# Kernel tuning notes

Measured on AMD Instinct MI355X. Metric: run time of the kernel, lower is better.

## Reference

```python
import jax, jax.numpy as jnp
import numpy as np

V, DH, E, KV = 30, 512, 256, 128  # vocab, decoder hidden, embed (=2*KV, tied), key/value dim
B, T, L = 256, 800, 300
SOS = 0


def _lstm_cell(x, h, c, w_ih, w_hh, b_ih, b_hh):
    g = x @ w_ih.T + b_ih + h @ w_hh.T + b_hh
    i, f, gg, o = jnp.split(g, 4, axis=-1)
    i, f, o = jax.nn.sigmoid(i), jax.nn.sigmoid(f), jax.nn.sigmoid(o)
    c2 = f * c + i * jnp.tanh(gg)
    return o * jnp.tanh(c2), c2


def setup_inputs() -> dict:
    key = jax.random.key(0)
    ks = jax.random.split(key, 12)
    emb = 0.1 * jax.random.normal(ks[0], (V, E), jnp.float32)
    emb = emb.at[0].set(0.0)  # padding_idx=0
    return {
        "key_enc": jax.random.normal(ks[1], (B, T, KV), jnp.float32),
        "value": jax.random.normal(ks[2], (B, T, KV), jnp.float32),
        "encoder_len": jax.random.randint(ks[3], (B,), 100, T + 1, jnp.int32),
        "y": jax.random.randint(ks[4], (B, L), 0, V, jnp.int64),
        "embedding": emb,  # also the tied character_prob weight (V, 2*KV)
        "w_ih1": 0.05 * jax.random.normal(ks[5], (4 * DH, E + KV), jnp.float32),
        "w_hh1": 0.05 * jax.random.normal(ks[6], (4 * DH, DH), jnp.float32),
        "b_ih1": jnp.zeros((4 * DH,), jnp.float32),
        "b_hh1": jnp.zeros((4 * DH,), jnp.float32),
        "w_ih2": 0.05 * jax.random.normal(ks[7], (4 * KV, DH), jnp.float32),
        "w_hh2": 0.05 * jax.random.normal(ks[8], (4 * KV, KV), jnp.float32),
        "b_ih2": jnp.zeros((4 * KV,), jnp.float32),
        "b_hh2": jnp.zeros((4 * KV,), jnp.float32),
        "out_bias": jnp.zeros((V,), jnp.float32),
    }


def reference(key_enc, value, encoder_len, y, embedding,
              w_ih1, w_hh1, b_ih1, b_hh1, w_ih2, w_hh2, b_ih2, b_hh2, out_bias):
    Bb, Tt, _ = key_enc.shape
    max_len = y.shape[1]
    valid = jnp.arange(Tt)[None, :] < encoder_len[:, None]  # (B, T)

    # teacher-forced embeddings: <sos> then y[:, :-1]
    sos = jnp.broadcast_to(embedding[SOS], (Bb, E))
    embeds = jnp.concatenate([sos[:, None, :], embedding[y[:, :-1]]], axis=1)  # (B, L, E)
    embeds = jnp.transpose(embeds, (1, 0, 2))  # (L, B, E)

    z1 = jnp.zeros((Bb, DH), key_enc.dtype)
    z2 = jnp.zeros((Bb, KV), key_enc.dtype)
    init = (z1, z1, z2, z2, value[:, 0, :])

    def step(carry, emb):
        h1, c1, h2, c2, ctx = carry
        x = jnp.concatenate([emb, ctx], axis=1)
        h1, c1 = _lstm_cell(x, h1, c1, w_ih1, w_hh1, b_ih1, b_hh1)
        h2, c2 = _lstm_cell(h1, h2, c2, w_ih2, w_hh2, b_ih2, b_hh2)
        q = h2  # (B, KV)
        energy = jnp.einsum('btk,bk->bt', key_enc, q)
        energy = jnp.where(valid, energy, -1e9)
        attn = jax.nn.softmax(energy, axis=-1)
        ctx = jnp.einsum('bt,btk->bk', attn, value)
        pred = jnp.concatenate([q, ctx], axis=1) @ embedding.T + out_bias  # tied weights
        return (h1, c1, h2, c2, ctx), (pred, attn[0])

    _, (preds, attn_plot) = jax.lax.scan(step, init, embeds)
    predictions = jnp.transpose(preds, (1, 0, 2))  # (B, L, V)
    return predictions, attn_plot  # attn_plot: (L, T)
```

## Files before the change

kernel.cpp:

```cpp
#include <hip/hip_runtime.h>
#include <cstddef>

#define NV   30
#define NDH  512
#define NE   256
#define NKV  128
#define NB   256
#define NT   800
#define NL   300
#define NKX  896

#define PRED_SIZE (NB*NL*NV)

typedef float v4f __attribute__((ext_vector_type(4)));
typedef short bf16x8 __attribute__((ext_vector_type(8)));
typedef unsigned short ushort_t;

#define OFF_C1   0
#define OFF_C2   131072
#define OFF_H2F  163840
#define OFF_XB   196608
#define OFF_XH2  458752
#define OFF_WF   524288
#define OFF_WF2  2359296
#define OFF_BS1  2686976
#define OFF_BS2  2689024

#define WF_PL   ((size_t)128*28*64*8)
#define WF2_PL  ((size_t)32*20*64*8)

struct DecParams {
  const float* key; const float* val; const int* elen; const int* y;
  const float* emb;
  const float* wi1; const float* wh1; const float* bi1; const float* bh1;
  const float* wi2; const float* wh2; const float* bi2; const float* bh2;
  const float* ob;
  float* out; float* ws;
};

__device__ __forceinline__ float sigm(float x)  { return 1.0f/(1.0f + __expf(-x)); }
__device__ __forceinline__ float tanh_f(float x){ return 1.0f - 2.0f/(__expf(2.0f*x)+1.0f); }

__device__ __forceinline__ ushort_t bf16_rne(float x){
  union { float f; unsigned u; } v; v.f = x;
  unsigned r = v.u + 0x7FFFu + ((v.u >> 16) & 1u);
  return (ushort_t)(r >> 16);
}
__device__ __forceinline__ float bf16_to_f(ushort_t h){
  union { float f; unsigned u; } v; v.u = ((unsigned)h) << 16;
  return v.f;
}

__global__ void __launch_bounds__(256)
k_init(DecParams P)
{
  P.ws[blockIdx.x * 256 + threadIdx.x] = 0.0f;
}

__global__ void __launch_bounds__(256)
k_initX(DecParams P)
{
  const int b = blockIdx.x, tid = threadIdx.x;
  if (tid < 128) {
    ushort_t* xbh = (ushort_t*)(P.ws + OFF_XB);
    ushort_t* xbl = xbh + (size_t)256*1024;
    const float v = P.val[(size_t)b*NT*NKV + tid];
    const ushort_t hi = bf16_rne(v);
    const ushort_t lo = bf16_rne(v - bf16_to_f(hi));
    xbh[(size_t)b*1024 + 256 + tid] = hi;
    xbl[(size_t)b*1024 + 256 + tid] = lo;
  }
}

__global__ void __launch_bounds__(256)
k_initW(DecParams P)
{
  const int r = blockIdx.x;
  const int tid = threadIdx.x;
  ushort_t* wf = (ushort_t*)(P.ws + OFF_WF);
  const int rt = r >> 4;
#pragma unroll
  for (int i = 0; i < 4; ++i) {
    const int k = i*256 + tid;
    if (k < NKX) {
      const float w = (k < 384) ? P.wi1[(size_t)r*384 + k]
                                : P.wh1[(size_t)r*512 + (k - 384)];
      const ushort_t hi = bf16_rne(w);
      const ushort_t lo = bf16_rne(w - bf16_to_f(hi));
      const int kc = k >> 5;
      const int lane = (r & 15) | (((k >> 3) & 3) << 4);
      const int e = k & 7;
      const size_t base = ((((size_t)rt)*28 + kc)*64 + lane)*8 + e;
      wf[base] = hi;
      wf[WF_PL + base] = lo;
    }
  }
  if (tid == 0) P.ws[OFF_BS1 + r] = P.bi1[r] + P.bh1[r];
}

__global__ void __launch_bounds__(256)
k_initW2(DecParams P)
{
  const int r = blockIdx.x;
  const int tid = threadIdx.x;
  ushort_t* wf = (ushort_t*)(P.ws + OFF_WF2);
  const int rt = r >> 4;
#pragma unroll
  for (int i = 0; i < 3; ++i) {
    const int k = i*256 + tid;
    if (k < 640) {
      const float w = (k < 512) ? P.wi2[(size_t)r*512 + k]
                                : P.wh2[(size_t)r*128 + (k - 512)];
      const ushort_t hi = bf16_rne(w);
      const ushort_t lo = bf16_rne(w - bf16_to_f(hi));
      const int kc = k >> 5;
      const int lane = (r & 15) | (((k >> 3) & 3) << 4);
      const int e = k & 7;
      const size_t base = ((((size_t)rt)*20 + kc)*64 + lane)*8 + e;
      wf[base] = hi;
      wf[WF2_PL + base] = lo;
    }
  }
  if (tid == 0) P.ws[OFF_BS2 + r] = P.bi2[r] + P.bh2[r];
}

__global__ void __launch_bounds__(256)
k_stepA(DecParams P)
{
  __shared__ ushort_t xs[2][32][136];
  __shared__ float gbuf[4][16][33];
  const int tid = threadIdx.x, bid = blockIdx.x;
  const int mt = bid & 31, nt = bid >> 5;
  const int b0 = nt * 32, j0 = mt * 16;
  const int w = tid >> 6, lane = tid & 63;
  const int rt16 = w*32 + mt;

  const ushort_t* Wf  = (const ushort_t*)(P.ws + OFF_WF);
  const ushort_t* XbH = (const ushort_t*)(P.ws + OFF_XB);
  const ushort_t* XbL = XbH + (size_t)256*1024;
  float* C1 = P.ws + OFF_C1;
  const float* BS1 = P.ws + OFF_BS1;

  v4f acc[2] = {(v4f)0.0f, (v4f)0.0f};
  const int srow = tid >> 3, sk = (tid & 7) * 16;
  const int lr = lane & 15, lk8 = (lane >> 4) * 8;

#pragma unroll 1
  for (int p = 0; p < 7; ++p) {
    __syncthreads();
    {
      const ushort_t* s0 = XbH + (size_t)(b0 + srow)*1024 + p*128 + sk;
      const ushort_t* s1 = XbL + (size_t)(b0 + srow)*1024 + p*128 + sk;
      *(bf16x8*)&xs[0][srow][sk]     = ((const bf16x8*)s0)[0];
      *(bf16x8*)&xs[0][srow][sk + 8] = ((const bf16x8*)s0)[1];
      *(bf16x8*)&xs[1][srow][sk]     = ((const bf16x8*)s1)[0];
      *(bf16x8*)&xs[1][srow][sk + 8] = ((const bf16x8*)s1)[1];
    }
    __syncthreads();
#pragma unroll
    for (int kc2 = 0; kc2 < 4; ++kc2) {
      const int kcg = p*4 + kc2;
      bf16x8 ah = *(const bf16x8*)(Wf + (((size_t)rt16*28 + kcg)*64 + lane)*8);
      bf16x8 al = *(const bf16x8*)(Wf + WF_PL + (((size_t)rt16*28 + kcg)*64 + lane)*8);
      const int lk = kc2*32 + lk8;
#pragma unroll
      for (int ct = 0; ct < 2; ++ct) {
        bf16x8 bh = *(const bf16x8*)&xs[0][ct*16 + lr][lk];
        bf16x8 bl = *(const bf16x8*)&xs[1][ct*16 + lr][lk];
        acc[ct] = __builtin_amdgcn_mfma_f32_16x16x32_bf16(ah, bh, acc[ct], 0, 0, 0);
        acc[ct] = __builtin_amdgcn_mfma_f32_16x16x32_bf16(ah, bl, acc[ct], 0, 0, 0);
        acc[ct] = __builtin_amdgcn_mfma_f32_16x16x32_bf16(al, bh, acc[ct], 0, 0, 0);
      }
    }
  }
  __syncthreads();
  const int rg = (lane >> 4) * 4;
#pragma unroll
  for (int ct = 0; ct < 2; ++ct)
#pragma unroll
    for (int j = 0; j < 4; ++j)
      gbuf[w][rg + j][ct*16 + lr] = acc[ct][j];
  __syncthreads();

  ushort_t* XbHw = (ushort_t*)(P.ws + OFF_XB);
  ushort_t* XbLw = XbHw + (size_t)256*1024;
#pragma unroll
  for (int it = 0; it < 2; ++it) {
    const int idx = it*256 + tid;
    const int jj = idx >> 5, bq = idx & 31;
    const int jg = j0 + jj, b = b0 + bq;
    const float iv = sigm (gbuf[0][jj][bq] + BS1[       jg]);
    const float fv = sigm (gbuf[1][jj][bq] + BS1[ 512 + jg]);
    const float gv = tanh_f(gbuf[2][jj][bq] + BS1[1024 + jg]);
    const float ov = sigm (gbuf[3][jj][bq] + BS1[1536 + jg]);
    const float cn = fv * C1[(size_t)jg*256 + b] + iv * gv;
    C1[(size_t)jg*256 + b] = cn;
    const float h = ov * tanh_f(cn);
    const ushort_t hi = bf16_rne(h);
    const ushort_t lo = bf16_rne(h - bf16_to_f(hi));
    XbHw[(size_t)b*1024 + 384 + jg] = hi;
    XbLw[(size_t)b*1024 + 384 + jg] = lo;
  }
}

__global__ void __launch_bounds__(256)
k_stepB(DecParams P, int t)
{
  __shared__ ushort_t xs[2][32][136];
  __shared__ float gbuf[4][16][33];
  const int tid = threadIdx.x, bid = blockIdx.x;
  const int mt = bid & 7, nt = bid >> 3;
  const int b0 = nt * 32, j0 = mt * 16;
  const int w = tid >> 6, lane = tid & 63;
  const int rt16 = w*8 + mt;

  const ushort_t* Wf2 = (const ushort_t*)(P.ws + OFF_WF2);
  const ushort_t* XbH = (const ushort_t*)(P.ws + OFF_XB);
  const ushort_t* XbL = XbH + (size_t)256*1024;
  const ushort_t* XH2 = (const ushort_t*)(P.ws + OFF_XH2);
  float* C2  = P.ws + OFF_C2;
  float* H2f = P.ws + OFF_H2F;
  const float* BS2 = P.ws + OFF_BS2;
  const int pp = t & 1, pn = (t + 1) & 1;

  v4f acc[2] = {(v4f)0.0f, (v4f)0.0f};
  const int srow = tid >> 3, sk = (tid & 7) * 16;
  const int lr = lane & 15, lk8 = (lane >> 4) * 8;

#pragma unroll 1
  for (int p = 0; p < 5; ++p) {
    __syncthreads();
    {
      const ushort_t* s0;
      const ushort_t* s1;
      if (p < 4) {
        s0 = XbH + (size_t)(b0 + srow)*1024 + 384 + p*128 + sk;
        s1 = XbL + (size_t)(b0 + srow)*1024 + 384 + p*128 + sk;
      } else {
        s0 = XH2 + ((size_t)(pp*2 + 0)*256 + b0 + srow)*128 + sk;
        s1 = XH2 + ((size_t)(pp*2 + 1)*256 + b0 + srow)*128 + sk;
      }
      *(bf16x8*)&xs[0][srow][sk]     = ((const bf16x8*)s0)[0];
      *(bf16x8*)&xs[0][srow][sk + 8] = ((const bf16x8*)s0)[1];
      *(bf16x8*)&xs[1][srow][sk]     = ((const bf16x8*)s1)[0];
      *(bf16x8*)&xs[1][srow][sk + 8] = ((const bf16x8*)s1)[1];
    }
    __syncthreads();
#pragma unroll
    for (int kc2 = 0; kc2 < 4; ++kc2) {
      const int kcg = p*4 + kc2;
      bf16x8 ah = *(const bf16x8*)(Wf2 + (((size_t)rt16*20 + kcg)*64 + lane)*8);
      bf16x8 al = *(const bf16x8*)(Wf2 + WF2_PL + (((size_t)rt16*20 + kcg)*64 + lane)*8);
      const int lk = kc2*32 + lk8;
#pragma unroll
      for (int ct = 0; ct < 2; ++ct) {
        bf16x8 bh = *(const bf16x8*)&xs[0][ct*16 + lr][lk];
        bf16x8 bl = *(const bf16x8*)&xs[1][ct*16 + lr][lk];
        acc[ct] = __builtin_amdgcn_mfma_f32_16x16x32_bf16(ah, bh, acc[ct], 0, 0, 0);
        acc[ct] = __builtin_amdgcn_mfma_f32_16x16x32_bf16(ah, bl, acc[ct], 0, 0, 0);
        acc[ct] = __builtin_amdgcn_mfma_f32_16x16x32_bf16(al, bh, acc[ct], 0, 0, 0);
      }
    }
  }
  __syncthreads();
  const int rg = (lane >> 4) * 4;
#pragma unroll
  for (int ct = 0; ct < 2; ++ct)
#pragma unroll
    for (int j = 0; j < 4; ++j)
      gbuf[w][rg + j][ct*16 + lr] = acc[ct][j];
  __syncthreads();

  ushort_t* XH2w = (ushort_t*)(P.ws + OFF_XH2);
#pragma unroll
  for (int it = 0; it < 2; ++it) {
    const int idx = it*256 + tid;
    const int jj = idx >> 5, bq = idx & 31;
    const int j2 = j0 + jj, b = b0 + bq;
    const float iv = sigm (gbuf[0][jj][bq] + BS2[      j2]);
    const float fv = sigm (gbuf[1][jj][bq] + BS2[128 + j2]);
    const float gv = tanh_f(gbuf[2][jj][bq] + BS2[256 + j2]);
    const float ov = sigm (gbuf[3][jj][bq] + BS2[384 + j2]);
    const float cn = fv * C2[(size_t)j2*256 + b] + iv * gv;
    C2[(size_t)j2*256 + b] = cn;
    const float h = ov * tanh_f(cn);
    H2f[(size_t)b*128 + j2] = h;
    const ushort_t hi = bf16_rne(h);
    const ushort_t lo = bf16_rne(h - bf16_to_f(hi));
    XH2w[((size_t)(pn*2 + 0)*256 + b)*128 + j2] = hi;
    XH2w[((size_t)(pn*2 + 1)*256 + b)*128 + j2] = lo;
  }
}

__global__ void __launch_bounds__(512)
k_stepC(DecParams P, int t)
{
  __shared__ float e[NT];
  __shared__ float qc[256];
  __shared__ float red[16];
  __shared__ float ctxp[16][132];

  const int tid = threadIdx.x;
  const int b = blockIdx.x;
  const int len = P.elen[b];
  const float* H2f = P.ws + OFF_H2F;
  ushort_t* xbh = (ushort_t*)(P.ws + OFF_XB);
  ushort_t* xbl = xbh + (size_t)256*1024;

  if (tid < 128) qc[tid] = H2f[(size_t)b*128 + tid];
  __syncthreads();

  const int lg = tid & 15, grp = tid >> 4;
  const v4f qa = *(const v4f*)&qc[lg*8];
  const v4f qb = *(const v4f*)&qc[lg*8 + 4];
  const v4f* kb = (const v4f*)(P.key + (size_t)b*NT*NKV);
#pragma unroll 1
  for (int s = 0; s < 13; ++s) {
    const int ta = s*64 + grp, tb = ta + 32;
    float pa = 0.0f, pb = 0.0f;
    if (ta < len) {
      v4f k0 = kb[(size_t)ta*32 + lg*2], k1 = kb[(size_t)ta*32 + lg*2 + 1];
      v4f d = k0*qa + k1*qb; pa = d[0]+d[1]+d[2]+d[3];
    }
    if (tb < len) {
      v4f k0 = kb[(size_t)tb*32 + lg*2], k1 = kb[(size_t)tb*32 + lg*2 + 1];
      v4f d = k0*qa + k1*qb; pb = d[0]+d[1]+d[2]+d[3];
    }
    pa += __shfl_xor(pa, 1); pb += __shfl_xor(pb, 1);
    pa += __shfl_xor(pa, 2); pb += __shfl_xor(pb, 2);
    pa += __shfl_xor(pa, 4); pb += __shfl_xor(pb, 4);
    pa += __shfl_xor(pa, 8); pb += __shfl_xor(pb, 8);
    if (lg == 0) {
      if (ta < len) e[ta] = pa;
      if (tb < len) e[tb] = pb;
    }
  }
  for (int tt = len + tid; tt < NT; tt += 512) e[tt] = -1e9f;
  __syncthreads();

  const int wid = tid >> 6;
  const float x0 = e[tid];
  const float x1 = (tid < NT - 512) ? e[512 + tid] : -3.0e38f;
  float m = fmaxf(x0, x1);
  m = fmaxf(m, __shfl_xor(m, 1));  m = fmaxf(m, __shfl_xor(m, 2));
  m = fmaxf(m, __shfl_xor(m, 4));  m = fmaxf(m, __shfl_xor(m, 8));
  m = fmaxf(m, __shfl_xor(m, 16)); m = fmaxf(m, __shfl_xor(m, 32));
  if ((tid & 63) == 0) red[wid] = m;
  __syncthreads();
  m = red[0];
#pragma unroll
  for (int i = 1; i < 8; ++i) m = fmaxf(m, red[i]);
  const float p0 = __expf(x0 - m);
  const float p1 = (tid < NT - 512) ? __expf(x1 - m) : 0.0f;
  float ss = p0 + p1;
  ss += __shfl_xor(ss, 1);  ss += __shfl_xor(ss, 2);  ss += __shfl_xor(ss, 4);
  ss += __shfl_xor(ss, 8);  ss += __shfl_xor(ss, 16); ss += __shfl_xor(ss, 32);
  if ((tid & 63) == 0) red[8 + wid] = ss;
  __syncthreads();
  float S = red[8];
#pragma unroll
  for (int i = 1; i < 8; ++i) S += red[8 + i];
  const float inv = 1.0f / S;
  e[tid] = p0 * inv;
  if (tid < NT - 512) e[512 + tid] = p1 * inv;
  if (b == 0) {
    P.out[PRED_SIZE + (size_t)t*NT + tid] = p0 * inv;
    if (tid < NT - 512) P.out[PRED_SIZE + (size_t)t*NT + 512 + tid] = p1 * inv;
  }
  __syncthreads();

  {
    const int kq = tid & 31, tq = tid >> 5;
    const v4f* vb = (const v4f*)(P.val + (size_t)b*NT*NKV);
    v4f a4 = (v4f)0.0f, a42 = (v4f)0.0f;
    int tt = tq;
    for (; tt + 16 < len; tt += 32) {
      a4  += e[tt]      * vb[(size_t)tt*32 + kq];
      a42 += e[tt + 16] * vb[(size_t)(tt + 16)*32 + kq];
    }
    if (tt < len) a4 += e[tt] * vb[(size_t)tt*32 + kq];
    a4 += a42;
    *(v4f*)&ctxp[tq][kq*4] = a4;
  }
  __syncthreads();
  if (tid < 128) {
    const int k = tid;
    float c = 0.0f;
#pragma unroll
    for (int r = 0; r < 16; ++r) c += ctxp[r][k];
    qc[128 + k] = c;
    const ushort_t hi = bf16_rne(c);
    const ushort_t lo = bf16_rne(c - bf16_to_f(hi));
    xbh[(size_t)b*1024 + 256 + k] = hi;
    xbl[(size_t)b*1024 + 256 + k] = lo;
  }
  __syncthreads();

  {
    const int vv = tid >> 4, lg16 = tid & 15;
    if (vv < NV) {
      const v4f* er = (const v4f*)(P.emb + (size_t)vv*NE + lg16*16);
      const v4f* qr = (const v4f*)&qc[lg16*16];
      v4f s4 = er[0]*qr[0] + er[1]*qr[1] + er[2]*qr[2] + er[3]*qr[3];
      float p = s4[0] + s4[1] + s4[2] + s4[3];
      p += __shfl_xor(p, 1); p += __shfl_xor(p, 2);
      p += __shfl_xor(p, 4); p += __shfl_xor(p, 8);
      if (lg16 == 0) P.out[((size_t)b*NL + t)*NV + vv] = p + P.ob[vv];
    }
  }

  if (tid < 256) {
    const int tok = P.y[(size_t)b*NL + t];
    const float x = P.emb[(size_t)tok*NE + tid];
    const ushort_t hi = bf16_rne(x);
    const ushort_t lo = bf16_rne(x - bf16_to_f(hi));
    xbh[(size_t)b*1024 + tid] = hi;
    xbl[(size_t)b*1024 + tid] = lo;
  }
}

extern "C" void kernel_launch(void* const* d_in, const int* in_sizes, int n_in,
                              void* d_out, int out_size, void* d_ws, size_t ws_size,
                              hipStream_t stream) {
  (void)in_sizes; (void)n_in; (void)out_size; (void)ws_size;
  DecParams P;
  P.key  = (const float*)d_in[0];
  P.val  = (const float*)d_in[1];
  P.elen = (const int*)d_in[2];
  P.y    = (const int*)d_in[3];
  P.emb  = (const float*)d_in[4];
  P.wi1  = (const float*)d_in[5];
  P.wh1  = (const float*)d_in[6];
  P.bi1  = (const float*)d_in[7];
  P.bh1  = (const float*)d_in[8];
  P.wi2  = (const float*)d_in[9];
  P.wh2  = (const float*)d_in[10];
  P.bi2  = (const float*)d_in[11];
  P.bh2  = (const float*)d_in[12];
  P.ob   = (const float*)d_in[13];
  P.out  = (float*)d_out;
  P.ws   = (float*)d_ws;

  hipLaunchKernelGGL(k_init,   dim3(2048), dim3(256), 0, stream, P);
  hipLaunchKernelGGL(k_initX,  dim3(256),  dim3(256), 0, stream, P);
  hipLaunchKernelGGL(k_initW,  dim3(2048), dim3(256), 0, stream, P);
  hipLaunchKernelGGL(k_initW2, dim3(512),  dim3(256), 0, stream, P);
  for (int t = 0; t < NL; ++t) {
    hipLaunchKernelGGL(k_stepA, dim3(256), dim3(256), 0, stream, P);
    hipLaunchKernelGGL(k_stepB, dim3(64),  dim3(256), 0, stream, P, t);
    hipLaunchKernelGGL(k_stepC, dim3(NB),  dim3(512), 0, stream, P, t);
  }
}
```

Before: 15.61 ms.

## Fuse per-step kernels into a persistent kernel with grid barriers

Replaces the 900 per-timestep launches of three kernels with one persistent kernel that loops over timesteps and separates the LSTM1, LSTM2 and attention phases with a software grid barrier. The workspace layout is split into separate embed/context and double-buffered h1/h2 buffers so phases can read the previous step's state. Blocks grow to 512 threads, with each wave owning one column tile. The aim is to remove launch overhead and inter-kernel gaps, at the cost of atomic spin-barrier latency, a timeout fallback that flags failure, and the risk of deadlock if the computed grid is not fully co-resident.

After: 53.87 ms. 3.45x slower.

```diff
diff --git a/kernel.cpp b/kernel.cpp
--- a/kernel.cpp
+++ b/kernel.cpp
@@ -19,12 +19,14 @@
 #define OFF_C1   0
 #define OFF_C2   131072
 #define OFF_H2F  163840
-#define OFF_XB   196608
-#define OFF_XH2  458752
-#define OFF_WF   524288
-#define OFF_WF2  2359296
-#define OFF_BS1  2686976
-#define OFF_BS2  2689024
+#define OFF_XEC  196608
+#define OFF_XH1  294912
+#define OFF_XH2  557056
+#define OFF_BAR  622592
+#define OFF_WF   622848
+#define OFF_WF2  2457856
+#define OFF_BS1  2785536
+#define OFF_BS2  2787584
 
 #define WF_PL   ((size_t)128*28*64*8)
 #define WF2_PL  ((size_t)32*20*64*8)
@@ -51,6 +53,32 @@
   return v.f;
 }
 
+__device__ __forceinline__ void gridbar(int* bar, int G)
+{
+  __syncthreads();
+  if (threadIdx.x == 0) {
+    __threadfence_system();
+    const int g = __hip_atomic_load(&bar[1], __ATOMIC_RELAXED, __HIP_MEMORY_SCOPE_SYSTEM);
+    const int v = __hip_atomic_fetch_add(&bar[0], 1, __ATOMIC_ACQ_REL, __HIP_MEMORY_SCOPE_SYSTEM);
+    if (v == G - 1) {
+      __hip_atomic_store(&bar[0], 0, __ATOMIC_RELAXED, __HIP_MEMORY_SCOPE_SYSTEM);
+      __hip_atomic_fetch_add(&bar[1], 1, __ATOMIC_ACQ_REL, __HIP_MEMORY_SCOPE_SYSTEM);
+    } else {
+      long spins = 0;
+      while (__hip_atomic_load(&bar[1], __ATOMIC_ACQUIRE, __HIP_MEMORY_SCOPE_SYSTEM) == g) {
+        __builtin_amdgcn_s_sleep(8);
+        if (++spins > (1L << 20)) {
+          __hip_atomic_store(&bar[2], 1, __ATOMIC_RELAXED, __HIP_MEMORY_SCOPE_SYSTEM);
+          break;
+        }
+        if (__hip_atomic_load(&bar[2], __ATOMIC_RELAXED, __HIP_MEMORY_SCOPE_SYSTEM)) break;
+      }
+    }
+    __threadfence_system();
+  }
+  __syncthreads();
+}
+
 __global__ void __launch_bounds__(256)
 k_init(DecParams P)
 {
@@ -62,13 +90,12 @@
 {
   const int b = blockIdx.x, tid = threadIdx.x;
   if (tid < 128) {
-    ushort_t* xbh = (ushort_t*)(P.ws + OFF_XB);
-    ushort_t* xbl = xbh + (size_t)256*1024;
+    ushort_t* xec = (ushort_t*)(P.ws + OFF_XEC);
     const float v = P.val[(size_t)b*NT*NKV + tid];
     const ushort_t hi = bf16_rne(v);
     const ushort_t lo = bf16_rne(v - bf16_to_f(hi));
-    xbh[(size_t)b*1024 + 256 + tid] = hi;
-    xbl[(size_t)b*1024 + 256 + tid] = lo;
+    xec[((size_t)0*256 + b)*384 + 256 + tid] = hi;
+    xec[((size_t)1*256 + b)*384 + 256 + tid] = lo;
   }
 }
 
@@ -124,298 +151,286 @@
   if (tid == 0) P.ws[OFF_BS2 + r] = P.bi2[r] + P.bh2[r];
 }
 
-__global__ void __launch_bounds__(256)
-k_stepA(DecParams P)
-{
-  __shared__ ushort_t xs[2][32][136];
-  __shared__ float gbuf[4][16][33];
-  const int tid = threadIdx.x, bid = blockIdx.x;
-  const int mt = bid & 31, nt = bid >> 5;
-  const int b0 = nt * 32, j0 = mt * 16;
+union SMem {
+  struct { ushort_t xs[2][32][136]; float gbuf[4][16][33]; } ab;
+  struct { float e[NT]; float qc[256]; float red[16]; float ctxp[16][132]; } c;
+};
+
+__global__ void __launch_bounds__(512)
+k_persist(DecParams P, int G)
+{
+  __shared__ SMem sm;
+  const int tid = threadIdx.x;
+  const int bid = blockIdx.x;
   const int w = tid >> 6, lane = tid & 63;
-  const int rt16 = w*32 + mt;
-
-  const ushort_t* Wf  = (const ushort_t*)(P.ws + OFF_WF);
-  const ushort_t* XbH = (const ushort_t*)(P.ws + OFF_XB);
-  const ushort_t* XbL = XbH + (size_t)256*1024;
-  float* C1 = P.ws + OFF_C1;
-  const float* BS1 = P.ws + OFF_BS1;
-
-  v4f acc[2] = {(v4f)0.0f, (v4f)0.0f};
-  const int srow = tid >> 3, sk = (tid & 7) * 16;
   const int lr = lane & 15, lk8 = (lane >> 4) * 8;
-
-#pragma unroll 1
-  for (int p = 0; p < 7; ++p) {
-    __syncthreads();
-    {
-      const ushort_t* s0 = XbH + (size_t)(b0 + srow)*1024 + p*128 + sk;
-      const ushort_t* s1 = XbL + (size_t)(b0 + srow)*1024 + p*128 + sk;
-      *(bf16x8*)&xs[0][srow][sk]     = ((const bf16x8*)s0)[0];
-      *(bf16x8*)&xs[0][srow][sk + 8] = ((const bf16x8*)s0)[1];
-      *(bf16x8*)&xs[1][srow][sk]     = ((const bf16x8*)s1)[0];
-      *(bf16x8*)&xs[1][srow][sk + 8] = ((const bf16x8*)s1)[1];
-    }
-    __syncthreads();
-#pragma unroll
-    for (int kc2 = 0; kc2 < 4; ++kc2) {
-      const int kcg = p*4 + kc2;
-      bf16x8 ah = *(const bf16x8*)(Wf + (((size_t)rt16*28 + kcg)*64 + lane)*8);
-      bf16x8 al = *(const bf16x8*)(Wf + WF_PL + (((size_t)rt16*28 + kcg)*64 + lane)*8);
-      const int lk = kc2*32 + lk8;
-#pragma unroll
-      for (int ct = 0; ct < 2; ++ct) {
-        bf16x8 bh = *(const bf16x8*)&xs[0][ct*16 + lr][lk];
-        bf16x8 bl = *(const bf16x8*)&xs[1][ct*16 + lr][lk];
-        acc[ct] = __builtin_amdgcn_mfma_f32_16x16x32_bf16(ah, bh, acc[ct], 0, 0, 0);
-        acc[ct] = __builtin_amdgcn_mfma_f32_16x16x32_bf16(ah, bl, acc[ct], 0, 0, 0);
-        acc[ct] = __builtin_amdgcn_mfma_f32_16x16x32_bf16(al, bh, acc[ct], 0, 0, 0);
-      }
-    }
-  }
-  __syncthreads();
-  const int rg = (lane >> 4) * 4;
-#pragma unroll
-  for (int ct = 0; ct < 2; ++ct)
-#pragma unroll
-    for (int j = 0; j < 4; ++j)
-      gbuf[w][rg + j][ct*16 + lr] = acc[ct][j];
-  __syncthreads();
-
-  ushort_t* XbHw = (ushort_t*)(P.ws + OFF_XB);
-  ushort_t* XbLw = XbHw + (size_t)256*1024;
-#pragma unroll
-  for (int it = 0; it < 2; ++it) {
-    const int idx = it*256 + tid;
-    const int jj = idx >> 5, bq = idx & 31;
-    const int jg = j0 + jj, b = b0 + bq;
-    const float iv = sigm (gbuf[0][jj][bq] + BS1[       jg]);
-    const float fv = sigm (gbuf[1][jj][bq] + BS1[ 512 + jg]);
-    const float gv = tanh_f(gbuf[2][jj][bq] + BS1[1024 + jg]);
-    const float ov = sigm (gbuf[3][jj][bq] + BS1[1536 + jg]);
-    const float cn = fv * C1[(size_t)jg*256 + b] + iv * gv;
-    C1[(size_t)jg*256 + b] = cn;
-    const float h = ov * tanh_f(cn);
-    const ushort_t hi = bf16_rne(h);
-    const ushort_t lo = bf16_rne(h - bf16_to_f(hi));
-    XbHw[(size_t)b*1024 + 384 + jg] = hi;
-    XbLw[(size_t)b*1024 + 384 + jg] = lo;
-  }
-}
-
-__global__ void __launch_bounds__(256)
-k_stepB(DecParams P, int t)
-{
-  __shared__ ushort_t xs[2][32][136];
-  __shared__ float gbuf[4][16][33];
-  const int tid = threadIdx.x, bid = blockIdx.x;
-  const int mt = bid & 7, nt = bid >> 3;
-  const int b0 = nt * 32, j0 = mt * 16;
-  const int w = tid >> 6, lane = tid & 63;
-  const int rt16 = w*8 + mt;
-
-  const ushort_t* Wf2 = (const ushort_t*)(P.ws + OFF_WF2);
-  const ushort_t* XbH = (const ushort_t*)(P.ws + OFF_XB);
-  const ushort_t* XbL = XbH + (size_t)256*1024;
-  const ushort_t* XH2 = (const ushort_t*)(P.ws + OFF_XH2);
-  float* C2  = P.ws + OFF_C2;
-  float* H2f = P.ws + OFF_H2F;
-  const float* BS2 = P.ws + OFF_BS2;
-  const int pp = t & 1, pn = (t + 1) & 1;
-
-  v4f acc[2] = {(v4f)0.0f, (v4f)0.0f};
-  const int srow = tid >> 3, sk = (tid & 7) * 16;
-  const int lr = lane & 15, lk8 = (lane >> 4) * 8;
-
-#pragma unroll 1
-  for (int p = 0; p < 5; ++p) {
-    __syncthreads();
-    {
-      const ushort_t* s0;
-      const ushort_t* s1;
-      if (p < 4) {
-        s0 = XbH + (size_t)(b0 + srow)*1024 + 384 + p*128 + sk;
-        s1 = XbL + (size_t)(b0 + srow)*1024 + 384 + p*128 + sk;
-      } else {
-        s0 = XH2 + ((size_t)(pp*2 + 0)*256 + b0 + srow)*128 + sk;
-        s1 = XH2 + ((size_t)(pp*2 + 1)*256 + b0 + srow)*128 + sk;
-      }
-      *(bf16x8*)&xs[0][srow][sk]     = ((const bf16x8*)s0)[0];
-      *(bf16x8*)&xs[0][srow][sk + 8] = ((const bf16x8*)s0)[1];
-      *(bf16x8*)&xs[1][srow][sk]     = ((const bf16x8*)s1)[0];
-      *(bf16x8*)&xs[1][srow][sk + 8] = ((const bf16x8*)s1)[1];
-    }
-    __syncthreads();
-#pragma unroll
-    for (int kc2 = 0; kc2 < 4; ++kc2) {
-      const int kcg = p*4 + kc2;
-      bf16x8 ah = *(const bf16x8*)(Wf2 + (((size_t)rt16*20 + kcg)*64 + lane)*8);
-      bf16x8 al = *(const bf16x8*)(Wf2 + WF2_PL + (((size_t)rt16*20 + kcg)*64 + lane)*8);
-      const int lk = kc2*32 + lk8;
-#pragma unroll
-      for (int ct = 0; ct < 2; ++ct) {
-        bf16x8 bh = *(const bf16x8*)&xs[0][ct*16 + lr][lk];
-        bf16x8 bl = *(const bf16x8*)&xs[1][ct*16 + lr][lk];
-        acc[ct] = __builtin_amdgcn_mfma_f32_16x16x32_bf16(ah, bh, acc[ct], 0, 0, 0);
-        acc[ct] = __builtin_amdgcn_mfma_f32_16x16x32_bf16(ah, bl, acc[ct], 0, 0, 0);
-        acc[ct] = __builtin_amdgcn_mfma_f32_16x16x32_bf16(al, bh, acc[ct], 0, 0, 0);
-      }
-    }
-  }
-  __syncthreads();
-  const int rg = (lane >> 4) * 4;
-#pragma unroll
-  for (int ct = 0; ct < 2; ++ct)
-#pragma unroll
-    for (int j = 0; j < 4; ++j)
-      gbuf[w][rg + j][ct*16 + lr] = acc[ct][j];
-  __syncthreads();
-
-  ushort_t* XH2w = (ushort_t*)(P.ws + OFF_XH2);
-#pragma unroll
-  for (int it = 0; it < 2; ++it) {
-    const int idx = it*256 + tid;
-    const int jj = idx >> 5, bq = idx & 31;
-    const int j2 = j0 + jj, b = b0 + bq;
-    const float iv = sigm (gbuf[0][jj][bq] + BS2[      j2]);
-    const float fv = sigm (gbuf[1][jj][bq] + BS2[128 + j2]);
-    const float gv = tanh_f(gbuf[2][jj][bq] + BS2[256 + j2]);
-    const float ov = sigm (gbuf[3][jj][bq] + BS2[384 + j2]);
-    const float cn = fv * C2[(size_t)j2*256 + b] + iv * gv;
-    C2[(size_t)j2*256 + b] = cn;
-    const float h = ov * tanh_f(cn);
-    H2f[(size_t)b*128 + j2] = h;
-    const ushort_t hi = bf16_rne(h);
-    const ushort_t lo = bf16_rne(h - bf16_to_f(hi));
-    XH2w[((size_t)(pn*2 + 0)*256 + b)*128 + j2] = hi;
-    XH2w[((size_t)(pn*2 + 1)*256 + b)*128 + j2] = lo;
-  }
-}
-
-__global__ void __launch_bounds__(512)
-k_stepC(DecParams P, int t)
-{
-  __shared__ float e[NT];
-  __shared__ float qc[256];
-  __shared__ float red[16];
-  __shared__ float ctxp[16][132];
-
-  const int tid = threadIdx.x;
-  const int b = blockIdx.x;
-  const int len = P.elen[b];
-  const float* H2f = P.ws + OFF_H2F;
-  ushort_t* xbh = (ushort_t*)(P.ws + OFF_XB);
-  ushort_t* xbl = xbh + (size_t)256*1024;
-
-  if (tid < 128) qc[tid] = H2f[(size_t)b*128 + tid];
-  __syncthreads();
-
-  const int lg = tid & 15, grp = tid >> 4;
-  const v4f qa = *(const v4f*)&qc[lg*8];
-  const v4f qb = *(const v4f*)&qc[lg*8 + 4];
-  const v4f* kb = (const v4f*)(P.key + (size_t)b*NT*NKV);
-#pragma unroll 1
-  for (int s = 0; s < 13; ++s) {
-    const int ta = s*64 + grp, tb = ta + 32;
-    float pa = 0.0f, pb = 0.0f;
-    if (ta < len) {
-      v4f k0 = kb[(size_t)ta*32 + lg*2], k1 = kb[(size_t)ta*32 + lg*2 + 1];
-      v4f d = k0*qa + k1*qb; pa = d[0]+d[1]+d[2]+d[3];
-    }
-    if (tb < len) {
-      v4f k0 = kb[(size_t)tb*32 + lg*2], k1 = kb[(size_t)tb*32 + lg*2 + 1];
-      v4f d = k0*qa + k1*qb; pb = d[0]+d[1]+d[2]+d[3];
-    }
-    pa += __shfl_xor(pa, 1); pb += __shfl_xor(pb, 1);
-    pa += __shfl_xor(pa, 2); pb += __shfl_xor(pb, 2);
-    pa += __shfl_xor(pa, 4); pb += __shfl_xor(pb, 4);
-    pa += __shfl_xor(pa, 8); pb += __shfl_xor(pb, 8);
-    if (lg == 0) {
-      if (ta < len) e[ta] = pa;
-      if (tb < len) e[tb] = pb;
-    }
-  }
-  for (int tt = len + tid; tt < NT; tt += 512) e[tt] = -1e9f;
-  __syncthreads();
-
-  const int wid = tid >> 6;
-  const float x0 = e[tid];
-  const float x1 = (tid < NT - 512) ? e[512 + tid] : -3.0e38f;
-  float m = fmaxf(x0, x1);
-  m = fmaxf(m, __shfl_xor(m, 1));  m = fmaxf(m, __shfl_xor(m, 2));
-  m = fmaxf(m, __shfl_xor(m, 4));  m = fmaxf(m, __shfl_xor(m, 8));
-  m = fmaxf(m, __shfl_xor(m, 16)); m = fmaxf(m, __shfl_xor(m, 32));
-  if ((tid & 63) == 0) red[wid] = m;
-  __syncthreads();
-  m = red[0];
-#pragma unroll
-  for (int i = 1; i < 8; ++i) m = fmaxf(m, red[i]);
-  const float p0 = __expf(x0 - m);
-  const float p1 = (tid < NT - 512) ? __expf(x1 - m) : 0.0f;
-  float ss = p0 + p1;
-  ss += __shfl_xor(ss, 1);  ss += __shfl_xor(ss, 2);  ss += __shfl_xor(ss, 4);
-  ss += __shfl_xor(ss, 8);  ss += __shfl_xor(ss, 16); ss += __shfl_xor(ss, 32);
-  if ((tid & 63) == 0) red[8 + wid] = ss;
-  __syncthreads();
-  float S = red[8];
-#pragma unroll
-  for (int i = 1; i < 8; ++i) S += red[8 + i];
-  const float inv = 1.0f / S;
-  e[tid] = p0 * inv;
-  if (tid < NT - 512) e[512 + tid] = p1 * inv;
-  if (b == 0) {
-    P.out[PRED_SIZE + (size_t)t*NT + tid] = p0 * inv;
-    if (tid < NT - 512) P.out[PRED_SIZE + (size_t)t*NT + 512 + tid] = p1 * inv;
-  }
-  __syncthreads();
-
-  {
-    const int kq = tid & 31, tq = tid >> 5;
-    const v4f* vb = (const v4f*)(P.val + (size_t)b*NT*NKV);
-    v4f a4 = (v4f)0.0f, a42 = (v4f)0.0f;
-    int tt = tq;
-    for (; tt + 16 < len; tt += 32) {
-      a4  += e[tt]      * vb[(size_t)tt*32 + kq];
-      a42 += e[tt + 16] * vb[(size_t)(tt + 16)*32 + kq];
-    }
-    if (tt < len) a4 += e[tt] * vb[(size_t)tt*32 + kq];
-    a4 += a42;
-    *(v4f*)&ctxp[tq][kq*4] = a4;
-  }
-  __syncthreads();
-  if (tid < 128) {
-    const int k = tid;
-    float c = 0.0f;
-#pragma unroll
-    for (int r = 0; r < 16; ++r) c += ctxp[r][k];
-    qc[128 + k] = c;
-    const ushort_t hi = bf16_rne(c);
-    const ushort_t lo = bf16_rne(c - bf16_to_f(hi));
-    xbh[(size_t)b*1024 + 256 + k] = hi;
-    xbl[(size_t)b*1024 + 256 + k] = lo;
-  }
-  __syncthreads();
-
-  {
-    const int vv = tid >> 4, lg16 = tid & 15;
-    if (vv < NV) {
-      const v4f* er = (const v4f*)(P.emb + (size_t)vv*NE + lg16*16);
-      const v4f* qr = (const v4f*)&qc[lg16*16];
-      v4f s4 = er[0]*qr[0] + er[1]*qr[1] + er[2]*qr[2] + er[3]*qr[3];
-      float p = s4[0] + s4[1] + s4[2] + s4[3];
-      p += __shfl_xor(p, 1); p += __shfl_xor(p, 2);
-      p += __shfl_xor(p, 4); p += __shfl_xor(p, 8);
-      if (lg16 == 0) P.out[((size_t)b*NL + t)*NV + vv] = p + P.ob[vv];
-    }
-  }
-
-  if (tid < 256) {
-    const int tok = P.y[(size_t)b*NL + t];
-    const float x = P.emb[(size_t)tok*NE + tid];
-    const ushort_t hi = bf16_rne(x);
-    const ushort_t lo = bf16_rne(x - bf16_to_f(hi));
-    xbh[(size_t)b*1024 + tid] = hi;
-    xbl[(size_t)b*1024 + tid] = lo;
+  const int srow = tid >> 4, sk = (tid & 15) * 8;
+
+  float* ws = P.ws;
+  int* bar = (int*)(ws + OFF_BAR);
+  const ushort_t* Wf  = (const ushort_t*)(ws + OFF_WF);
+  const ushort_t* Wf2 = (const ushort_t*)(ws + OFF_WF2);
+  ushort_t* XEC = (ushort_t*)(ws + OFF_XEC);
+  ushort_t* XH1 = (ushort_t*)(ws + OFF_XH1);
+  ushort_t* XH2 = (ushort_t*)(ws + OFF_XH2);
+  float* C1  = ws + OFF_C1;
+  float* C2  = ws + OFF_C2;
+  float* H2f = ws + OFF_H2F;
+  const float* BS1 = ws + OFF_BS1;
+  const float* BS2 = ws + OFF_BS2;
+
+#pragma unroll 1
+  for (int t = 0; t < NL; ++t) {
+    const int cur = t & 1, nxt = (t + 1) & 1;
+
+#pragma unroll 1
+    for (int tileA = bid; tileA < 256; tileA += G) {
+      const int mt = tileA & 31, nt = tileA >> 5;
+      const int b0 = nt * 32, j0 = mt * 16;
+      const int g = w >> 1, ct = w & 1;
+      const int rt16 = g*32 + mt;
+      v4f acc = (v4f)0.0f;
+
+#pragma unroll 1
+      for (int p = 0; p < 7; ++p) {
+        __syncthreads();
+        {
+          const ushort_t *s0, *s1;
+          if (p < 3) {
+            s0 = XEC + ((size_t)(0*256 + b0 + srow))*384 + p*128 + sk;
+            s1 = XEC + ((size_t)(1*256 + b0 + srow))*384 + p*128 + sk;
+          } else {
+            s0 = XH1 + (((size_t)cur*2 + 0)*256 + b0 + srow)*512 + (p-3)*128 + sk;
+            s1 = XH1 + (((size_t)cur*2 + 1)*256 + b0 + srow)*512 + (p-3)*128 + sk;
+          }
+          *(bf16x8*)&sm.ab.xs[0][srow][sk] = *(const bf16x8*)s0;
+          *(bf16x8*)&sm.ab.xs[1][srow][sk] = *(const bf16x8*)s1;
+        }
+        __syncthreads();
+#pragma unroll
+        for (int kc2 = 0; kc2 < 4; ++kc2) {
+          const int kcg = p*4 + kc2;
+          bf16x8 ah = *(const bf16x8*)(Wf + (((size_t)rt16*28 + kcg)*64 + lane)*8);
+          bf16x8 al = *(const bf16x8*)(Wf + WF_PL + (((size_t)rt16*28 + kcg)*64 + lane)*8);
+          const int lk = kc2*32 + lk8;
+          bf16x8 bh = *(const bf16x8*)&sm.ab.xs[0][ct*16 + lr][lk];
+          bf16x8 bl = *(const bf16x8*)&sm.ab.xs[1][ct*16 + lr][lk];
+          acc = __builtin_amdgcn_mfma_f32_16x16x32_bf16(ah, bh, acc, 0, 0, 0);
+          acc = __builtin_amdgcn_mfma_f32_16x16x32_bf16(ah, bl, acc, 0, 0, 0);
+          acc = __builtin_amdgcn_mfma_f32_16x16x32_bf16(al, bh, acc, 0, 0, 0);
+        }
+      }
+      __syncthreads();
+      {
+        const int rg = (lane >> 4) * 4;
+#pragma unroll
+        for (int j = 0; j < 4; ++j) sm.ab.gbuf[g][rg + j][ct*16 + lr] = acc[j];
+      }
+      __syncthreads();
+      {
+        const int jj = tid >> 5, bq = tid & 31;
+        const int jg = j0 + jj, b = b0 + bq;
+        const float iv = sigm (sm.ab.gbuf[0][jj][bq] + BS1[       jg]);
+        const float fv = sigm (sm.ab.gbuf[1][jj][bq] + BS1[ 512 + jg]);
+        const float gv = tanh_f(sm.ab.gbuf[2][jj][bq] + BS1[1024 + jg]);
+        const float ov = sigm (sm.ab.gbuf[3][jj][bq] + BS1[1536 + jg]);
+        const float cn = fv * C1[(size_t)jg*256 + b] + iv * gv;
+        C1[(size_t)jg*256 + b] = cn;
+        const float h = ov * tanh_f(cn);
+        const ushort_t hi = bf16_rne(h);
+        const ushort_t lo = bf16_rne(h - bf16_to_f(hi));
+        XH1[(((size_t)nxt*2 + 0)*256 + b)*512 + jg] = hi;
+        XH1[(((size_t)nxt*2 + 1)*256 + b)*512 + jg] = lo;
+      }
+    }
+    gridbar(bar, G);
+
+#pragma unroll 1
+    for (int tileB = bid; tileB < 64; tileB += G) {
+      const int mt = tileB & 7, nt = tileB >> 3;
+      const int b0 = nt * 32, j0 = mt * 16;
+      const int g = w >> 1, ct = w & 1;
+      const int rt16 = g*8 + mt;
+      v4f acc = (v4f)0.0f;
+
+#pragma unroll 1
+      for (int p = 0; p < 5; ++p) {
+        __syncthreads();
+        {
+          const ushort_t *s0, *s1;
+          if (p < 4) {
+            s0 = XH1 + (((size_t)nxt*2 + 0)*256 + b0 + srow)*512 + p*128 + sk;
+            s1 = XH1 + (((size_t)nxt*2 + 1)*256 + b0 + srow)*512 + p*128 + sk;
+          } else {
+            s0 = XH2 + (((size_t)cur*2 + 0)*256 + b0 + srow)*128 + sk;
+            s1 = XH2 + (((size_t)cur*2 + 1)*256 + b0 + srow)*128 + sk;
+          }
+          *(bf16x8*)&sm.ab.xs[0][srow][sk] = *(const bf16x8*)s0;
+          *(bf16x8*)&sm.ab.xs[1][srow][sk] = *(const bf16x8*)s1;
+        }
+        __syncthreads();
+#pragma unroll
+        for (int kc2 = 0; kc2 < 4; ++kc2) {
+          const int kcg = p*4 + kc2;
+          bf16x8 ah = *(const bf16x8*)(Wf2 + (((size_t)rt16*20 + kcg)*64 + lane)*8);
+          bf16x8 al = *(const bf16x8*)(Wf2 + WF2_PL + (((size_t)rt16*20 + kcg)*64 + lane)*8);
+          const int lk = kc2*32 + lk8;
+          bf16x8 bh = *(const bf16x8*)&sm.ab.xs[0][ct*16 + lr][lk];
+          bf16x8 bl = *(const bf16x8*)&sm.ab.xs[1][ct*16 + lr][lk];
+          acc = __builtin_amdgcn_mfma_f32_16x16x32_bf16(ah, bh, acc, 0, 0, 0);
+          acc = __builtin_amdgcn_mfma_f32_16x16x32_bf16(ah, bl, acc, 0, 0, 0);
+          acc = __builtin_amdgcn_mfma_f32_16x16x32_bf16(al, bh, acc, 0, 0, 0);
+        }
+      }
+      __syncthreads();
+      {
+        const int rg = (lane >> 4) * 4;
+#pragma unroll
+        for (int j = 0; j < 4; ++j) sm.ab.gbuf[g][rg + j][ct*16 + lr] = acc[j];
+      }
+      __syncthreads();
+      {
+        const int jj = tid >> 5, bq = tid & 31;
+        const int j2 = j0 + jj, b = b0 + bq;
+        const float iv = sigm (sm.ab.gbuf[0][jj][bq] + BS2[      j2]);
+        const float fv = sigm (sm.ab.gbuf[1][jj][bq] + BS2[128 + j2]);
+        const float gv = tanh_f(sm.ab.gbuf[2][jj][bq] + BS2[256 + j2]);
+        const float ov = sigm (sm.ab.gbuf[3][jj][bq] + BS2[384 + j2]);
+        const float cn = fv * C2[(size_t)j2*256 + b] + iv * gv;
+        C2[(size_t)j2*256 + b] = cn;
+        const float h = ov * tanh_f(cn);
+        H2f[(size_t)b*128 + j2] = h;
+        const ushort_t hi = bf16_rne(h);
+        const ushort_t lo = bf16_rne(h - bf16_to_f(hi));
+        XH2[(((size_t)nxt*2 + 0)*256 + b)*128 + j2] = hi;
+        XH2[(((size_t)nxt*2 + 1)*256 + b)*128 + j2] = lo;
+      }
+    }
+    gridbar(bar, G);
+
+#pragma unroll 1
+    for (int b = bid; b < NB; b += G) {
+      __syncthreads();
+      const int len = P.elen[b];
+
+      if (tid < 128) sm.c.qc[tid] = H2f[(size_t)b*128 + tid];
+      __syncthreads();
+
+      const int lg = tid & 15, grp = tid >> 4;
+      const v4f qa = *(const v4f*)&sm.c.qc[lg*8];
+      const v4f qb = *(const v4f*)&sm.c.qc[lg*8 + 4];
+      const v4f* kb = (const v4f*)(P.key + (size_t)b*NT*NKV);
+#pragma unroll 1
+      for (int s = 0; s < 13; ++s) {
+        const int ta = s*64 + grp, tb = ta + 32;
+        float pa = 0.0f, pb = 0.0f;
+        if (ta < len) {
+          v4f k0 = kb[(size_t)ta*32 + lg*2], k1 = kb[(size_t)ta*32 + lg*2 + 1];
+          v4f d = k0*qa + k1*qb; pa = d[0]+d[1]+d[2]+d[3];
+        }
+        if (tb < len) {
+          v4f k0 = kb[(size_t)tb*32 + lg*2], k1 = kb[(size_t)tb*32 + lg*2 + 1];
+          v4f d = k0*qa + k1*qb; pb = d[0]+d[1]+d[2]+d[3];
+        }
+        pa += __shfl_xor(pa, 1); pb += __shfl_xor(pb, 1);
+        pa += __shfl_xor(pa, 2); pb += __shfl_xor(pb, 2);
+        pa += __shfl_xor(pa, 4); pb += __shfl_xor(pb, 4);
+        pa += __shfl_xor(pa, 8); pb += __shfl_xor(pb, 8);
+        if (lg == 0) {
+          if (ta < len) sm.c.e[ta] = pa;
+          if (tb < len) sm.c.e[tb] = pb;
+        }
+      }
+      for (int tt = len + tid; tt < NT; tt += 512) sm.c.e[tt] = -1e9f;
+      __syncthreads();
+
+      const int wid = tid >> 6;
+      const float x0 = sm.c.e[tid];
+      const float x1 = (tid < NT - 512) ? sm.c.e[512 + tid] : -3.0e38f;
+      float m = fmaxf(x0, x1);
+      m = fmaxf(m, __shfl_xor(m, 1));  m = fmaxf(m, __shfl_xor(m, 2));
+      m = fmaxf(m, __shfl_xor(m, 4));  m = fmaxf(m, __shfl_xor(m, 8));
+      m = fmaxf(m, __shfl_xor(m, 16)); m = fmaxf(m, __shfl_xor(m, 32));
+      if ((tid & 63) == 0) sm.c.red[wid] = m;
+      __syncthreads();
+      m = sm.c.red[0];
+#pragma unroll
+      for (int i = 1; i < 8; ++i) m = fmaxf(m, sm.c.red[i]);
+      const float p0 = __expf(x0 - m);
+      const float p1 = (tid < NT - 512) ? __expf(x1 - m) : 0.0f;
+      float ssum = p0 + p1;
+      ssum += __shfl_xor(ssum, 1);  ssum += __shfl_xor(ssum, 2);  ssum += __shfl_xor(ssum, 4);
+      ssum += __shfl_xor(ssum, 8);  ssum += __shfl_xor(ssum, 16); ssum += __shfl_xor(ssum, 32);
+      __syncthreads();
+      if ((tid & 63) == 0) sm.c.red[8 + wid] = ssum;
+      __syncthreads();
+      float S = sm.c.red[8];
+#pragma unroll
+      for (int i = 1; i < 8; ++i) S += sm.c.red[8 + i];
+      const float inv = 1.0f / S;
+      sm.c.e[tid] = p0 * inv;
+      if (tid < NT - 512) sm.c.e[512 + tid] = p1 * inv;
+      if (b == 0) {
+        P.out[PRED_SIZE + (size_t)t*NT + tid] = p0 * inv;
+        if (tid < NT - 512) P.out[PRED_SIZE + (size_t)t*NT + 512 + tid] = p1 * inv;
+      }
+      __syncthreads();
+
+      {
+        const int kq = tid & 31, tq = tid >> 5;
+        const v4f* vb = (const v4f*)(P.val + (size_t)b*NT*NKV);
+        v4f a4 = (v4f)0.0f, a42 = (v4f)0.0f;
+        int tt = tq;
+        for (; tt + 16 < len; tt += 32) {
+          a4  += sm.c.e[tt]      * vb[(size_t)tt*32 + kq];
+          a42 += sm.c.e[tt + 16] * vb[(size_t)(tt + 16)*32 + kq];
+        }
+        if (tt < len) a4 += sm.c.e[tt] * vb[(size_t)tt*32 + kq];
+        a4 += a42;
+        *(v4f*)&sm.c.ctxp[tq][kq*4] = a4;
+      }
+      __syncthreads();
+      if (tid < 128) {
+        const int k = tid;
+        float c = 0.0f;
+#pragma unroll
+        for (int r = 0; r < 16; ++r) c += sm.c.ctxp[r][k];
+        sm.c.qc[128 + k] = c;
+        const ushort_t hi = bf16_rne(c);
+        const ushort_t lo = bf16_rne(c - bf16_to_f(hi));
+        XEC[((size_t)0*256 + b)*384 + 256 + k] = hi;
+        XEC[((size_t)1*256 + b)*384 + 256 + k] = lo;
+      }
+      __syncthreads();
+
+      {
+        const int vv = tid >> 4, lg16 = tid & 15;
+        if (vv < NV) {
+          const v4f* er = (const v4f*)(P.emb + (size_t)vv*NE + lg16*16);
+          const v4f* qr = (const v4f*)&sm.c.qc[lg16*16];
+          v4f s4 = er[0]*qr[0] + er[1]*qr[1] + er[2]*qr[2] + er[3]*qr[3];
+          float p = s4[0] + s4[1] + s4[2] + s4[3];
+          p += __shfl_xor(p, 1); p += __shfl_xor(p, 2);
+          p += __shfl_xor(p, 4); p += __shfl_xor(p, 8);
+          if (lg16 == 0) P.out[((size_t)b*NL + t)*NV + vv] = p + P.ob[vv];
+        }
+      }
+
+      if (tid < 256) {
+        const int tok = P.y[(size_t)b*NL + t];
+        const float x = P.emb[(size_t)tok*NE + tid];
+        const ushort_t hi = bf16_rne(x);
+        const ushort_t lo = bf16_rne(x - bf16_to_f(hi));
+        XEC[((size_t)0*256 + b)*384 + tid] = hi;
+        XEC[((size_t)1*256 + b)*384 + tid] = lo;
+      }
+    }
+    gridbar(bar, G);
+  }
+
+  if (bid == 0 && tid == 0) {
+    if (__hip_atomic_load(&bar[2], __ATOMIC_RELAXED, __HIP_MEMORY_SCOPE_SYSTEM))
+      P.out[0] = 1.0e9f;
   }
 }
 
@@ -441,13 +456,19 @@
   P.out  = (float*)d_out;
   P.ws   = (float*)d_ws;
 
-  hipLaunchKernelGGL(k_init,   dim3(2048), dim3(256), 0, stream, P);
-  hipLaunchKernelGGL(k_initX,  dim3(256),  dim3(256), 0, stream, P);
-  hipLaunchKernelGGL(k_initW,  dim3(2048), dim3(256), 0, stream, P);
-  hipLaunchKernelGGL(k_initW2, dim3(512),  dim3(256), 0, stream, P);
-  for (int t = 0; t < NL; ++t) {
-    hipLaunchKernelGGL(k_stepA, dim3(256), dim3(256), 0, stream, P);
-    hipLaunchKernelGGL(k_stepB, dim3(64),  dim3(256), 0, stream, P, t);
-    hipLaunchKernelGGL(k_stepC, dim3(NB),  dim3(512), 0, stream, P, t);
-  }
-}
+  int perCU = 0;
+  hipOccupancyMaxActiveBlocksPerMultiprocessor(&perCU, (const void*)k_persist, 512, 0);
+  hipDeviceProp_t prop;
+  int dev = 0;
+  hipGetDevice(&dev);
+  hipGetDeviceProperties(&prop, dev);
+  int G = perCU * prop.multiProcessorCount;
+  if (G > NB) G = NB;
+  if (G < 1)  G = 1;
+
+  hipLaunchKernelGGL(k_init,    dim3(2433), dim3(256), 0, stream, P);
+  hipLaunchKernelGGL(k_initX,   dim3(256),  dim3(256), 0, stream, P);
+  hipLaunchKernelGGL(k_initW,   dim3(2048), dim3(256), 0, stream, P);
+  hipLaunchKernelGGL(k_initW2,  dim3(512),  dim3(256), 0, stream, P);
+  hipLaunchKernelGGL(k_persist, dim3(G),    dim3(512), 0, stream, P, G);
+}
```
